# Kernel tuning notes

Hardware: AMD Instinct MI355X
Metric: run time of the kernel (lower is better)

## Reference

```python
import math
import jax, jax.numpy as jnp
import numpy as np

D = 256      # embedding_dim (= internal_dim, downsample_rate 1)
H = 8        # num_heads
HD = D // H  # head_dim = 32
NTC = 16     # num_text_classes
NIMG = 4096  # image tokens (64x64)
N = NIMG + NTC
B = 2
NKE = 64     # num_k_exclude_rope


def _rope(x, freqs):
    # x: (b, h, n, c); freqs: (n, c//2, 2) = (cos, sin) of complex rotary factors
    b, h, n, c = x.shape
    xp = x.reshape(b, h, n, c // 2, 2)
    cos, sin = freqs[..., 0], freqs[..., 1]
    xr, xi = xp[..., 0], xp[..., 1]
    out_r = xr * cos - xi * sin
    out_i = xr * sin + xi * cos
    return jnp.stack([out_r, out_i], axis=-1).reshape(b, h, n, c)


def _sep_heads(x):
    b, n, c = x.shape
    return x.reshape(b, n, H, c // H).transpose(0, 2, 1, 3)  # (b,h,n,hd)


def setup_inputs() -> dict:
    key = jax.random.key(0)
    ks = jax.random.split(key, 14)
    s = 0.02
    # rotary factors: unit-norm cos/sin pairs
    ang_img = jax.random.uniform(ks[3], (NIMG, HD // 2)) * (2.0 * np.pi)
    ang_txt = jax.random.uniform(ks[4], (NTC, HD // 2)) * (2.0 * np.pi)
    return {
        "q": jax.random.normal(ks[0], (B, N, D), dtype=jnp.float32),
        "k": jax.random.normal(ks[1], (B, N, D), dtype=jnp.float32),
        "v": jax.random.normal(ks[2], (B, N, D), dtype=jnp.float32),
        "freqs_cis_img": jnp.stack([jnp.cos(ang_img), jnp.sin(ang_img)], axis=-1),
        "freqs_cis_txt": jnp.stack([jnp.cos(ang_txt), jnp.sin(ang_txt)], axis=-1),
        "Wq": jax.random.normal(ks[5], (D, D), dtype=jnp.float32) * s,
        "bq": jnp.zeros((D,), dtype=jnp.float32),
        "Wk": jax.random.normal(ks[6], (D, D), dtype=jnp.float32) * s,
        "bk": jnp.zeros((D,), dtype=jnp.float32),
        "Wv": jax.random.normal(ks[7], (D, D), dtype=jnp.float32) * s,
        "bv": jnp.zeros((D,), dtype=jnp.float32),
        "Wo": jax.random.normal(ks[8], (D, D), dtype=jnp.float32) * s,
        "bo": jnp.zeros((D,), dtype=jnp.float32),
        "num_k_exclude_rope": NKE,
    }


def reference(q, k, v, freqs_cis_img, freqs_cis_txt,
              Wq, bq, Wk, bk, Wv, bv, Wo, bo, num_k_exclude_rope):
    q = q @ Wq.T + bq
    k = k @ Wk.T + bk
    v = v @ Wv.T + bv
    q = _sep_heads(q)  # (b,h,n,hd)
    k = _sep_heads(k)
    v = _sep_heads(v)

    # split tokens into image / text regions, apply RoPE separately
    q_img, q_txt = q[:, :, :-NTC, :], q[:, :, -NTC:, :]
    k_img, k_txt = k[:, :, :-NTC, :], k[:, :, -NTC:, :]
    q_img = _rope(q_img, freqs_cis_img)
    k_img = _rope(k_img, freqs_cis_img)
    q_txt = _rope(q_txt, freqs_cis_txt)
    k_txt = _rope(k_txt, freqs_cis_txt)
    q = jnp.concatenate([q_img, q_txt], axis=-2)
    k = jnp.concatenate([k_img, k_txt], axis=-2)

    scale = 1.0 / math.sqrt(HD)
    nke = num_k_exclude_rope
    if nke > 0:
        k_td, k_mem = k[:, :, :-nke, :], k[:, :, -nke:, :]
        v_td, v_mem = v[:, :, :-nke, :], v[:, :, -nke:, :]
        attn = jax.nn.softmax(jnp.einsum('bhqd,bhkd->bhqk', q, k_td) * scale, axis=-1)
        out = jnp.einsum('bhqk,bhkd->bhqd', attn, v_td)
        attn_m = jax.nn.softmax(jnp.einsum('bhqd,bhkd->bhqk', q, k_mem) * scale, axis=-1)
        out = out + jnp.einsum('bhqk,bhkd->bhqd', attn_m, v_mem)
    else:
        attn = jax.nn.softmax(jnp.einsum('bhqd,bhkd->bhqk', q, k) * scale, axis=-1)
        out = jnp.einsum('bhqk,bhkd->bhqd', attn, v)

    b, h, n, hd = out.shape
    out = out.transpose(0, 2, 1, 3).reshape(b, n, h * hd)
    return out @ Wo.T + bo
```

## Files before the change

### kernel.cpp

```cpp
#include <hip/hip_runtime.h>
#include <hip/hip_bf16.h>

#define BN    4112
#define NKR   4160
#define BNP   4160
#define BB    2
#define HH    8
#define NIMG_ 4096
#define NMAIN 4048
#define MROWS 8224
#define QSCALE 0.25505402f

typedef __attribute__((ext_vector_type(8))) short short8;
typedef __attribute__((ext_vector_type(4))) float f32x4;
typedef __attribute__((ext_vector_type(16))) float f32x16;

__device__ __forceinline__ unsigned short f2bs(float x) { return __bfloat16_as_ushort(__float2bfloat16(x)); }
__device__ __forceinline__ unsigned pkbf(float a, float b) {
    __hip_bfloat162 h = __float22bfloat162_rn(make_float2(a, b));
    unsigned u; __builtin_memcpy(&u, &h, 4); return u;
}
__device__ __forceinline__ float fexp2(float x) {
#if __has_builtin(__builtin_amdgcn_exp2f)
    return __builtin_amdgcn_exp2f(x);
#else
    return exp2f(x);
#endif
}

__global__ __launch_bounds__(256)
void qkv_mfma(const float* __restrict__ Aq, const float* __restrict__ Ak, const float* __restrict__ Av,
              const float* __restrict__ Wq, const float* __restrict__ Wk, const float* __restrict__ Wv,
              const float* __restrict__ bq, const float* __restrict__ bk, const float* __restrict__ bv,
              short* __restrict__ Qr, short* __restrict__ Kr, short* __restrict__ Vt,
              const float* __restrict__ fimg, const float* __restrict__ ftxt)
{
    __shared__ __align__(16) short Ws[2][64][72];
    __shared__ __align__(16) short Ds[2][64][72];

    const int mode = blockIdx.z;
    const float* A    = (mode == 0) ? Aq : (mode == 1) ? Ak : Av;
    const float* W    = (mode == 0) ? Wq : (mode == 1) ? Wk : Wv;
    const float* bias = (mode == 0) ? bq : (mode == 1) ? bk : bv;

    const int t    = threadIdx.x;
    const int wave = t >> 6, lane = t & 63, q16 = lane & 15, quad = lane >> 4;
    const int f0 = blockIdx.x * 64;
    const int m0 = blockIdx.y * 64;
    const int sr = t >> 2, sc = (t & 3) * 16;
    const int arow = m0 + sr;
    const bool aval = arow < MROWS;
    const float* wp = W + (size_t)(f0 + sr) * 256 + sc;
    const float* ap = A + (size_t)(aval ? arow : 0) * 256 + sc;

    f32x4 acc[4] = {{0,0,0,0},{0,0,0,0},{0,0,0,0},{0,0,0,0}};

    uint4 wr0, wr1, dr0, dr1;
    {
        float4 a0 = *(const float4*)(wp),     a1 = *(const float4*)(wp + 4);
        float4 a2 = *(const float4*)(wp + 8), a3 = *(const float4*)(wp + 12);
        wr0 = uint4{pkbf(a0.x,a0.y), pkbf(a0.z,a0.w), pkbf(a1.x,a1.y), pkbf(a1.z,a1.w)};
        wr1 = uint4{pkbf(a2.x,a2.y), pkbf(a2.z,a2.w), pkbf(a3.x,a3.y), pkbf(a3.z,a3.w)};
        a0 = *(const float4*)(ap);     a1 = *(const float4*)(ap + 4);
        a2 = *(const float4*)(ap + 8); a3 = *(const float4*)(ap + 12);
        dr0 = uint4{pkbf(a0.x,a0.y), pkbf(a0.z,a0.w), pkbf(a1.x,a1.y), pkbf(a1.z,a1.w)};
        dr1 = uint4{pkbf(a2.x,a2.y), pkbf(a2.z,a2.w), pkbf(a3.x,a3.y), pkbf(a3.z,a3.w)};
    }
    *(uint4*)&Ws[0][sr][sc] = wr0; *(uint4*)&Ws[0][sr][sc + 8] = wr1;
    *(uint4*)&Ds[0][sr][sc] = dr0; *(uint4*)&Ds[0][sr][sc + 8] = dr1;
    __syncthreads();

    #pragma unroll
    for (int ki = 0; ki < 4; ++ki) {
        const int buf = ki & 1;
        if (ki < 3) {
            const int k1 = (ki + 1) * 64;
            float4 a0 = *(const float4*)(wp + k1),     a1 = *(const float4*)(wp + k1 + 4);
            float4 a2 = *(const float4*)(wp + k1 + 8), a3 = *(const float4*)(wp + k1 + 12);
            wr0 = uint4{pkbf(a0.x,a0.y), pkbf(a0.z,a0.w), pkbf(a1.x,a1.y), pkbf(a1.z,a1.w)};
            wr1 = uint4{pkbf(a2.x,a2.y), pkbf(a2.z,a2.w), pkbf(a3.x,a3.y), pkbf(a3.z,a3.w)};
            a0 = *(const float4*)(ap + k1);     a1 = *(const float4*)(ap + k1 + 4);
            a2 = *(const float4*)(ap + k1 + 8); a3 = *(const float4*)(ap + k1 + 12);
            dr0 = uint4{pkbf(a0.x,a0.y), pkbf(a0.z,a0.w), pkbf(a1.x,a1.y), pkbf(a1.z,a1.w)};
            dr1 = uint4{pkbf(a2.x,a2.y), pkbf(a2.z,a2.w), pkbf(a3.x,a3.y), pkbf(a3.z,a3.w)};
        }
        #pragma unroll
        for (int ks = 0; ks < 2; ++ks) {
            const short8 af = *(const short8*)&Ws[buf][wave * 16 + q16][ks * 32 + quad * 8];
            #pragma unroll
            for (int ct = 0; ct < 4; ++ct) {
                const short8 bf = *(const short8*)&Ds[buf][ct * 16 + q16][ks * 32 + quad * 8];
                acc[ct] = __builtin_amdgcn_mfma_f32_16x16x32_bf16(af, bf, acc[ct], 0, 0, 0);
            }
        }
        if (ki < 3) {
            *(uint4*)&Ws[buf ^ 1][sr][sc] = wr0; *(uint4*)&Ws[buf ^ 1][sr][sc + 8] = wr1;
            *(uint4*)&Ds[buf ^ 1][sr][sc] = dr0; *(uint4*)&Ds[buf ^ 1][sr][sc + 8] = dr1;
            __syncthreads();
        }
    }

    const int fbase = f0 + wave * 16 + quad * 4;
    const float4 bb = *(const float4*)(bias + fbase);
    float vs[4][4];
    #pragma unroll
    for (int ct = 0; ct < 4; ++ct) {
        int n = m0 + ct * 16 + q16;
        float v0 = acc[ct][0] + bb.x, v1 = acc[ct][1] + bb.y;
        float v2 = acc[ct][2] + bb.z, v3 = acc[ct][3] + bb.w;
        int b  = (n >= BN) ? 1 : 0;
        int nb = n - b * BN;
        if (mode < 2) {
            int j0 = (fbase & 31) >> 1;
            const float* fr = (nb < NIMG_) ? (fimg + ((size_t)nb * 16 + j0) * 2)
                                           : (ftxt + ((size_t)(nb - NIMG_) * 16 + j0) * 2);
            float4 cs = *(const float4*)fr;
            float r0 = v0 * cs.x - v1 * cs.y, i0 = v0 * cs.y + v1 * cs.x;
            float r1 = v2 * cs.z - v3 * cs.w, i1 = v2 * cs.w + v3 * cs.z;
            v0 = r0; v1 = i0; v2 = r1; v3 = i1;
        }
        if (mode == 2) {
            vs[ct][0] = v0; vs[ct][1] = v1; vs[ct][2] = v2; vs[ct][3] = v3;
            continue;
        }
        if (n >= MROWS) continue;
        const int h = (fbase >> 5) & 7, hd = fbase & 31;
        if (mode == 0) {
            unsigned short* op = (unsigned short*)Qr + (((size_t)(b * HH + h) * BN + nb) * 32 + hd);
            *(uint2*)op = uint2{pkbf(v0 * QSCALE, v1 * QSCALE), pkbf(v2 * QSCALE, v3 * QSCALE)};
        } else {
            int nk = nb + ((nb >= NMAIN) ? 48 : 0);
            unsigned short* op = (unsigned short*)Kr + (((size_t)(b * HH + h) * NKR + nk) * 32 + hd);
            *(uint2*)op = uint2{pkbf(v0, v1), pkbf(v2, v3)};
        }
    }

    if (mode == 2) {
        short (*Tr)[72] = Ds[0];
        const int fl = wave * 16 + quad * 4;
        #pragma unroll
        for (int ct = 0; ct < 4; ++ct) {
            const int nl = ct * 16 + q16;
            Tr[fl + 0][nl] = (short)f2bs(vs[ct][0]);
            Tr[fl + 1][nl] = (short)f2bs(vs[ct][1]);
            Tr[fl + 2][nl] = (short)f2bs(vs[ct][2]);
            Tr[fl + 3][nl] = (short)f2bs(vs[ct][3]);
        }
        __syncthreads();
        const int h0 = (f0 >> 5) & 7;
        #pragma unroll
        for (int ii = 0; ii < 2; ++ii) {
            const int r  = ii * 32 + (t >> 3);
            const int c8 = (t & 7) * 8;
            const int ng = m0 + c8;
            if (ng < MROWS) {
                uint4 val = *(const uint4*)&Tr[r][c8];
                int b  = (ng >= BN) ? 1 : 0;
                int nb = ng - b * BN;
                int nk = nb + ((nb >= NMAIN) ? 48 : 0);
                int h  = h0 + (r >> 5), hd = r & 31;
                unsigned short* op = (unsigned short*)Vt + ((size_t)(b * HH + h) * 32 + hd) * BNP + nk;
                *(uint4*)op = val;
            }
        }
    }

    if (blockIdx.x == 0 && blockIdx.y < 16 && t < 192) {
        const int bh = blockIdx.y;
        if (mode == 1) {
            short* base = Kr + (size_t)bh * NKR * 32 + (size_t)NMAIN * 32;
            *(uint4*)(base + t * 8) = uint4{0u, 0u, 0u, 0u};
        } else if (mode == 2) {
            short* base = Vt + (size_t)bh * 32 * BNP + (size_t)(t / 6) * BNP + NMAIN + (t % 6) * 8;
            *(uint4*)base = uint4{0u, 0u, 0u, 0u};
        }
    }
}

__global__ __launch_bounds__(256, 4)
void attn_mfma(const short* __restrict__ Qr, const short* __restrict__ Kr,
               const short* __restrict__ Vt, unsigned short* __restrict__ AO)
{
    __shared__ __align__(16) short Ks[2][2][64][40];
    __shared__ __align__(16) short Vs[2][2][32][72];

    const int t    = threadIdx.x;
    const int wave = t >> 6, lane = t & 63, q32 = lane & 31, hi = lane >> 5;
    const int grp  = wave >> 1, w2 = wave & 1;

    const int b_   = blockIdx.x;
    const int idx  = b_ >> 3;
    const int bh   = ((b_ & 7) << 1) + (idx >= 65 ? 1 : 0);
    const int bx   = idx - (idx >= 65 ? 65 : 0);

    const int q  = bx * 64 + w2 * 32 + q32;
    const int qc = (q < BN) ? q : (BN - 1);
    const short* qp = Qr + ((size_t)bh * BN + qc) * 32 + hi * 8;
    const short8 qf0 = *(const short8*)(qp);
    const short8 qf1 = *(const short8*)(qp + 16);

    f32x16 oAx = {0,0,0,0,0,0,0,0,0,0,0,0,0,0,0,0};
    f32x16 oAy = {0,0,0,0,0,0,0,0,0,0,0,0,0,0,0,0};
    f32x16 oBx = {0,0,0,0,0,0,0,0,0,0,0,0,0,0,0,0};
    const f32x16 z16 = {0,0,0,0,0,0,0,0,0,0,0,0,0,0,0,0};
    float LA = 0.f, LB = 0.f;

    const int tg = t & 127;
    const int kr = tg >> 2, kc = tg & 3;
    const int vr = tg >> 3, vc = tg & 7;
    const short* kg = Kr + (size_t)bh * NKR * 32 + (size_t)grp * 65536 + (size_t)kr * 32 + kc * 8;
    const short* vg = Vt + (size_t)bh * 32 * BNP + (size_t)vr * BNP + grp * 2048
                         + (vc >> 1) * 16 + (vc & 1) * 4;
    const int ntiles = 32 + grp;

    auto tile = [&](int buf, f32x16& ox, f32x16& oy, float& L) {
        const short8 kf00 = *(const short8*)&Ks[grp][buf][q32][hi * 8];
        const short8 kf01 = *(const short8*)&Ks[grp][buf][q32][16 + hi * 8];
        const short8 kf10 = *(const short8*)&Ks[grp][buf][32 + q32][hi * 8];
        const short8 kf11 = *(const short8*)&Ks[grp][buf][32 + q32][16 + hi * 8];
        f32x16 s0 = __builtin_amdgcn_mfma_f32_32x32x16_bf16(kf00, qf0, z16, 0, 0, 0);
        f32x16 s1 = __builtin_amdgcn_mfma_f32_32x32x16_bf16(kf10, qf0, z16, 0, 0, 0);
        s0 = __builtin_amdgcn_mfma_f32_32x32x16_bf16(kf01, qf1, s0, 0, 0, 0);
        s1 = __builtin_amdgcn_mfma_f32_32x32x16_bf16(kf11, qf1, s1, 0, 0, 0);
        float p0[16], p1[16];
        #pragma unroll
        for (int r = 0; r < 16; ++r) p0[r] = fexp2(s0[r]);
        #pragma unroll
        for (int r = 0; r < 16; ++r) p1[r] = fexp2(s1[r]);
        float l0 = (((p0[0]+p0[1])+(p0[2]+p0[3])) + ((p0[4]+p0[5])+(p0[6]+p0[7])))
                 + (((p0[8]+p0[9])+(p0[10]+p0[11])) + ((p0[12]+p0[13])+(p0[14]+p0[15])));
        float l1 = (((p1[0]+p1[1])+(p1[2]+p1[3])) + ((p1[4]+p1[5])+(p1[6]+p1[7])))
                 + (((p1[8]+p1[9])+(p1[10]+p1[11])) + ((p1[12]+p1[13])+(p1[14]+p1[15])));
        #pragma unroll
        for (int m = 0; m < 2; ++m) {
            uint4 pbu = uint4{pkbf(p0[8*m+0], p0[8*m+1]), pkbf(p0[8*m+2], p0[8*m+3]),
                              pkbf(p0[8*m+4], p0[8*m+5]), pkbf(p0[8*m+6], p0[8*m+7])};
            short8 pb; __builtin_memcpy(&pb, &pbu, 16);
            const short8 vf = *(const short8*)&Vs[grp][buf][q32][m * 16 + hi * 8];
            ox = __builtin_amdgcn_mfma_f32_32x32x16_bf16(vf, pb, ox, 0, 0, 0);
        }
        #pragma unroll
        for (int m = 0; m < 2; ++m) {
            uint4 pbu = uint4{pkbf(p1[8*m+0], p1[8*m+1]), pkbf(p1[8*m+2], p1[8*m+3]),
                              pkbf(p1[8*m+4], p1[8*m+5]), pkbf(p1[8*m+6], p1[8*m+7])};
            short8 pb; __builtin_memcpy(&pb, &pbu, 16);
            const short8 vf = *(const short8*)&Vs[grp][buf][q32][32 + m * 16 + hi * 8];
            oy = __builtin_amdgcn_mfma_f32_32x32x16_bf16(vf, pb, oy, 0, 0, 0);
        }
        L += l0 + l1;
    };

    *(uint4*)&Ks[grp][0][kr][kc * 8]      = *(const uint4*)(kg);
    *(uint4*)&Ks[grp][0][kr + 32][kc * 8] = *(const uint4*)(kg + 1024);
    {
        uint2 a0 = *(const uint2*)(vg),              b0 = *(const uint2*)(vg + 8);
        uint2 a1 = *(const uint2*)(vg + 16 * BNP),   b1 = *(const uint2*)(vg + 16 * BNP + 8);
        *(uint4*)&Vs[grp][0][vr][vc * 8]      = uint4{a0.x, a0.y, b0.x, b0.y};
        *(uint4*)&Vs[grp][0][vr + 16][vc * 8] = uint4{a1.x, a1.y, b1.x, b1.y};
    }
    __syncthreads();

    for (int it = 0; it < 33; ++it) {
        const int buf = it & 1;
        uint4 kreg0, kreg1; uint2 va0, vb0, va1, vb1;
        const bool pre = (it + 1) < ntiles;
        if (pre) {
            const short* kp = kg + (size_t)(it + 1) * 2048;
            kreg0 = *(const uint4*)(kp);
            kreg1 = *(const uint4*)(kp + 1024);
            const short* vp = vg + (it + 1) * 64;
            va0 = *(const uint2*)(vp);            vb0 = *(const uint2*)(vp + 8);
            va1 = *(const uint2*)(vp + 16 * BNP); vb1 = *(const uint2*)(vp + 16 * BNP + 8);
        }
        if (it < ntiles) {
            __builtin_amdgcn_s_setprio(1);
            if (grp == 0 || it < 32) tile(buf, oAx, oAy, LA);
            else                     tile(buf, oBx, oBx, LB);
            __builtin_amdgcn_s_setprio(0);
        }
        if (pre) {
            *(uint4*)&Ks[grp][buf ^ 1][kr][kc * 8]      = kreg0;
            *(uint4*)&Ks[grp][buf ^ 1][kr + 32][kc * 8] = kreg1;
            *(uint4*)&Vs[grp][buf ^ 1][vr][vc * 8]      = uint4{va0.x, va0.y, vb0.x, vb0.y};
            *(uint4*)&Vs[grp][buf ^ 1][vr + 16][vc * 8] = uint4{va1.x, va1.y, vb1.x, vb1.y};
        }
        __syncthreads();
    }

    f32x16 oA = oAx + oAy;
    f32x16 oB = oBx;

    LA += __shfl_xor(LA, 32);
    LB += __shfl_xor(LB, 32);

    float* ex = (float*)&Ks[0][0][0][0];
    const int slot = (w2 * 64 + lane) * 20;
    if (grp == 0) {
        #pragma unroll
        for (int i = 0; i < 4; ++i)
            *(f32x4*)(ex + slot + 4 * i) = f32x4{oA[4*i], oA[4*i+1], oA[4*i+2], oA[4*i+3]};
        ex[slot + 16] = LA;
    }
    __syncthreads();

    if (grp == 1 && q < BN) {
        float LT = LA + ex[slot + 16] - 48.f;
        const float iA = 1.f / LT, iB = 1.f / LB;
        const int b = bh >> 3, h = bh & 7;
        unsigned short* ap = AO + ((size_t)b * BN + q) * 256 + h * 32;
        #pragma unroll
        for (int k = 0; k < 4; ++k) {
            f32x4 a = *(const f32x4*)(ex + slot + 4 * k);
            float w0 = (oA[4*k+0] + a[0]) * iA + oB[4*k+0] * iB;
            float w1 = (oA[4*k+1] + a[1]) * iA + oB[4*k+1] * iB;
            float w2 = (oA[4*k+2] + a[2]) * iA + oB[4*k+2] * iB;
            float w3 = (oA[4*k+3] + a[3]) * iA + oB[4*k+3] * iB;
            *(uint2*)(ap + 8 * k + 4 * hi) = uint2{pkbf(w0, w1), pkbf(w2, w3)};
        }
    }
}

__global__ __launch_bounds__(256)
void gemm_out(const unsigned short* __restrict__ A, const float* __restrict__ W,
              const float* __restrict__ bias, float* __restrict__ out)
{
    __shared__ __align__(16) short Ws[2][64][72];
    __shared__ __align__(16) short Ds[2][64][72];
    const int t    = threadIdx.x;
    const int wave = t >> 6, lane = t & 63, q16 = lane & 15, quad = lane >> 4;
    const int f0 = blockIdx.x * 64, m0 = blockIdx.y * 64;
    const int sr = t >> 2, sc = (t & 3) * 16;
    const int arow = m0 + sr;
    const bool aval = arow < MROWS;
    const float* wp = W + (size_t)(f0 + sr) * 256 + sc;
    const unsigned short* ap = A + (size_t)(aval ? arow : 0) * 256 + sc;

    f32x4 acc[4] = {{0,0,0,0},{0,0,0,0},{0,0,0,0},{0,0,0,0}};

    uint4 wr0, wr1, dr0, dr1;
    {
        float4 a0 = *(const float4*)(wp),     a1 = *(const float4*)(wp + 4);
        float4 a2 = *(const float4*)(wp + 8), a3 = *(const float4*)(wp + 12);
        wr0 = uint4{pkbf(a0.x,a0.y), pkbf(a0.z,a0.w), pkbf(a1.x,a1.y), pkbf(a1.z,a1.w)};
        wr1 = uint4{pkbf(a2.x,a2.y), pkbf(a2.z,a2.w), pkbf(a3.x,a3.y), pkbf(a3.z,a3.w)};
        dr0 = *(const uint4*)(ap); dr1 = *(const uint4*)(ap + 8);
    }
    *(uint4*)&Ws[0][sr][sc] = wr0; *(uint4*)&Ws[0][sr][sc + 8] = wr1;
    *(uint4*)&Ds[0][sr][sc] = dr0; *(uint4*)&Ds[0][sr][sc + 8] = dr1;
    __syncthreads();

    #pragma unroll
    for (int ki = 0; ki < 4; ++ki) {
        const int buf = ki & 1;
        if (ki < 3) {
            const int k1 = (ki + 1) * 64;
            float4 a0 = *(const float4*)(wp + k1),     a1 = *(const float4*)(wp + k1 + 4);
            float4 a2 = *(const float4*)(wp + k1 + 8), a3 = *(const float4*)(wp + k1 + 12);
            wr0 = uint4{pkbf(a0.x,a0.y), pkbf(a0.z,a0.w), pkbf(a1.x,a1.y), pkbf(a1.z,a1.w)};
            wr1 = uint4{pkbf(a2.x,a2.y), pkbf(a2.z,a2.w), pkbf(a3.x,a3.y), pkbf(a3.z,a3.w)};
            dr0 = *(const uint4*)(ap + k1); dr1 = *(const uint4*)(ap + k1 + 8);
        }
        #pragma unroll
        for (int ks = 0; ks < 2; ++ks) {
            const short8 af = *(const short8*)&Ws[buf][wave * 16 + q16][ks * 32 + quad * 8];
            #pragma unroll
            for (int ct = 0; ct < 4; ++ct) {
                const short8 bf = *(const short8*)&Ds[buf][ct * 16 + q16][ks * 32 + quad * 8];
                acc[ct] = __builtin_amdgcn_mfma_f32_16x16x32_bf16(af, bf, acc[ct], 0, 0, 0);
            }
        }
        if (ki < 3) {
            *(uint4*)&Ws[buf ^ 1][sr][sc] = wr0; *(uint4*)&Ws[buf ^ 1][sr][sc + 8] = wr1;
            *(uint4*)&Ds[buf ^ 1][sr][sc] = dr0; *(uint4*)&Ds[buf ^ 1][sr][sc + 8] = dr1;
            __syncthreads();
        }
    }

    const int fbase = f0 + wave * 16 + quad * 4;
    const float4 bb = *(const float4*)(bias + fbase);
    #pragma unroll
    for (int ct = 0; ct < 4; ++ct) {
        int n = m0 + ct * 16 + q16;
        if (n >= MROWS) continue;
        float* op = out + (size_t)n * 256 + fbase;
        *(float4*)op = float4{acc[ct][0] + bb.x, acc[ct][1] + bb.y,
                              acc[ct][2] + bb.z, acc[ct][3] + bb.w};
    }
}

extern "C" void kernel_launch(void* const* d_in, const int* in_sizes, int n_in,
                              void* d_out, int out_size, void* d_ws, size_t ws_size,
                              hipStream_t stream)
{
    (void)in_sizes; (void)n_in; (void)out_size; (void)ws_size;
    const float* q    = (const float*)d_in[0];
    const float* k    = (const float*)d_in[1];
    const float* v    = (const float*)d_in[2];
    const float* fimg = (const float*)d_in[3];
    const float* ftxt = (const float*)d_in[4];
    const float* Wq   = (const float*)d_in[5];
    const float* bq   = (const float*)d_in[6];
    const float* Wk   = (const float*)d_in[7];
    const float* bk   = (const float*)d_in[8];
    const float* Wv   = (const float*)d_in[9];
    const float* bv   = (const float*)d_in[10];
    const float* Wo   = (const float*)d_in[11];
    const float* bo   = (const float*)d_in[12];

    char* w = (char*)d_ws;
    short*          Qr = (short*)(w);
    short*          Kr = (short*)(w + 4210688);
    short*          Vt = (short*)(w + 8470528);
    unsigned short* AO = (unsigned short*)(w + 12730368);

    qkv_mfma<<<dim3(4, 129, 3), 256, 0, stream>>>(q, k, v, Wq, Wk, Wv, bq, bk, bv,
                                                  Qr, Kr, Vt, fimg, ftxt);
    attn_mfma<<<dim3(1040), 256, 0, stream>>>(Qr, Kr, Vt, AO);
    gemm_out<<<dim3(4, 129), 256, 0, stream>>>(AO, Wo, bo, (float*)d_out);
}
```

Measured before the change: 193.0 us.

## Give each wave private single-buffered K/V tiles and drop per-iteration block barriers

```diff
diff --git a/kernel.cpp b/kernel.cpp
--- a/kernel.cpp
+++ b/kernel.cpp
@@ -181,43 +181,61 @@
 void attn_mfma(const short* __restrict__ Qr, const short* __restrict__ Kr,
                const short* __restrict__ Vt, unsigned short* __restrict__ AO)
 {
-    __shared__ __align__(16) short Ks[2][2][64][40];
-    __shared__ __align__(16) short Vs[2][2][32][72];
+    __shared__ __align__(16) short Ks[4][64][40];
+    __shared__ __align__(16) short Vs[4][32][72];
 
     const int t    = threadIdx.x;
     const int wave = t >> 6, lane = t & 63, q32 = lane & 31, hi = lane >> 5;
-    const int grp  = wave >> 1, w2 = wave & 1;
+    const int grp  = wave & 1;
+    const int qg   = wave >> 1;
 
     const int b_   = blockIdx.x;
     const int idx  = b_ >> 3;
     const int bh   = ((b_ & 7) << 1) + (idx >= 65 ? 1 : 0);
     const int bx   = idx - (idx >= 65 ? 65 : 0);
 
-    const int q  = bx * 64 + w2 * 32 + q32;
+    const int q  = bx * 64 + qg * 32 + q32;
     const int qc = (q < BN) ? q : (BN - 1);
     const short* qp = Qr + ((size_t)bh * BN + qc) * 32 + hi * 8;
     const short8 qf0 = *(const short8*)(qp);
     const short8 qf1 = *(const short8*)(qp + 16);
 
-    f32x16 oAx = {0,0,0,0,0,0,0,0,0,0,0,0,0,0,0,0};
-    f32x16 oAy = {0,0,0,0,0,0,0,0,0,0,0,0,0,0,0,0};
-    f32x16 oBx = {0,0,0,0,0,0,0,0,0,0,0,0,0,0,0,0};
+    f32x16 oA = {0,0,0,0,0,0,0,0,0,0,0,0,0,0,0,0};
+    f32x16 oB = {0,0,0,0,0,0,0,0,0,0,0,0,0,0,0,0};
     const f32x16 z16 = {0,0,0,0,0,0,0,0,0,0,0,0,0,0,0,0};
     float LA = 0.f, LB = 0.f;
 
-    const int tg = t & 127;
-    const int kr = tg >> 2, kc = tg & 3;
-    const int vr = tg >> 3, vc = tg & 7;
-    const short* kg = Kr + (size_t)bh * NKR * 32 + (size_t)grp * 65536 + (size_t)kr * 32 + kc * 8;
-    const short* vg = Vt + (size_t)bh * 32 * BNP + (size_t)vr * BNP + grp * 2048
-                         + (vc >> 1) * 16 + (vc & 1) * 4;
-    const int ntiles = 32 + grp;
-
-    auto tile = [&](int buf, f32x16& ox, f32x16& oy, float& L) {
-        const short8 kf00 = *(const short8*)&Ks[grp][buf][q32][hi * 8];
-        const short8 kf01 = *(const short8*)&Ks[grp][buf][q32][16 + hi * 8];
-        const short8 kf10 = *(const short8*)&Ks[grp][buf][32 + q32][hi * 8];
-        const short8 kf11 = *(const short8*)&Ks[grp][buf][32 + q32][16 + hi * 8];
+    const int krow = lane >> 1, khalf = lane & 1;
+    const int vrow = lane >> 2, vseg = lane & 3;
+    const short* kgb = Kr + (size_t)bh * NKR * 32 + (size_t)grp * 65536
+                          + (size_t)krow * 32 + khalf * 16;
+    const short* vgb = Vt + (size_t)bh * 32 * BNP + (size_t)vrow * BNP + grp * 2048 + vseg * 16;
+
+    short (*KsW)[40] = Ks[wave];
+    short (*VsW)[72] = Vs[wave];
+
+    auto commit = [&](uint4 k0, uint4 k1, uint4 k2, uint4 k3,
+                      uint4 vl0, uint4 vh0, uint4 vl1, uint4 vh1) {
+        *(uint4*)&KsW[krow][khalf * 16]          = k0;
+        *(uint4*)&KsW[krow][khalf * 16 + 8]      = k1;
+        *(uint4*)&KsW[krow + 32][khalf * 16]     = k2;
+        *(uint4*)&KsW[krow + 32][khalf * 16 + 8] = k3;
+        *(uint4*)&VsW[vrow][vseg * 16]           = uint4{vl0.x, vl0.y, vh0.x, vh0.y};
+        *(uint4*)&VsW[vrow][vseg * 16 + 8]       = uint4{vl0.z, vl0.w, vh0.z, vh0.w};
+        *(uint4*)&VsW[vrow + 16][vseg * 16]      = uint4{vl1.x, vl1.y, vh1.x, vh1.y};
+        *(uint4*)&VsW[vrow + 16][vseg * 16 + 8]  = uint4{vl1.z, vl1.w, vh1.z, vh1.w};
+    };
+
+    auto tileC = [&](f32x16& o, float& L) {
+        const short8 kf00 = *(const short8*)&KsW[q32][hi * 8];
+        const short8 kf01 = *(const short8*)&KsW[q32][16 + hi * 8];
+        const short8 kf10 = *(const short8*)&KsW[32 + q32][hi * 8];
+        const short8 kf11 = *(const short8*)&KsW[32 + q32][16 + hi * 8];
+        const short8 vf0 = *(const short8*)&VsW[q32][hi * 8];
+        const short8 vf1 = *(const short8*)&VsW[q32][16 + hi * 8];
+        const short8 vf2 = *(const short8*)&VsW[q32][32 + hi * 8];
+        const short8 vf3 = *(const short8*)&VsW[q32][48 + hi * 8];
+        __builtin_amdgcn_s_setprio(1);
         f32x16 s0 = __builtin_amdgcn_mfma_f32_32x32x16_bf16(kf00, qf0, z16, 0, 0, 0);
         f32x16 s1 = __builtin_amdgcn_mfma_f32_32x32x16_bf16(kf10, qf0, z16, 0, 0, 0);
         s0 = __builtin_amdgcn_mfma_f32_32x32x16_bf16(kf01, qf1, s0, 0, 0, 0);
@@ -231,86 +249,79 @@
                  + (((p0[8]+p0[9])+(p0[10]+p0[11])) + ((p0[12]+p0[13])+(p0[14]+p0[15])));
         float l1 = (((p1[0]+p1[1])+(p1[2]+p1[3])) + ((p1[4]+p1[5])+(p1[6]+p1[7])))
                  + (((p1[8]+p1[9])+(p1[10]+p1[11])) + ((p1[12]+p1[13])+(p1[14]+p1[15])));
-        #pragma unroll
-        for (int m = 0; m < 2; ++m) {
-            uint4 pbu = uint4{pkbf(p0[8*m+0], p0[8*m+1]), pkbf(p0[8*m+2], p0[8*m+3]),
-                              pkbf(p0[8*m+4], p0[8*m+5]), pkbf(p0[8*m+6], p0[8*m+7])};
+        {
+            uint4 pbu = uint4{pkbf(p0[0], p0[1]), pkbf(p0[2], p0[3]),
+                              pkbf(p0[4], p0[5]), pkbf(p0[6], p0[7])};
             short8 pb; __builtin_memcpy(&pb, &pbu, 16);
-            const short8 vf = *(const short8*)&Vs[grp][buf][q32][m * 16 + hi * 8];
-            ox = __builtin_amdgcn_mfma_f32_32x32x16_bf16(vf, pb, ox, 0, 0, 0);
-        }
-        #pragma unroll
-        for (int m = 0; m < 2; ++m) {
-            uint4 pbu = uint4{pkbf(p1[8*m+0], p1[8*m+1]), pkbf(p1[8*m+2], p1[8*m+3]),
-                              pkbf(p1[8*m+4], p1[8*m+5]), pkbf(p1[8*m+6], p1[8*m+7])};
+            o = __builtin_amdgcn_mfma_f32_32x32x16_bf16(vf0, pb, o, 0, 0, 0);
+        }
+        {
+            uint4 pbu = uint4{pkbf(p0[8], p0[9]),  pkbf(p0[10], p0[11]),
+                              pkbf(p0[12], p0[13]), pkbf(p0[14], p0[15])};
             short8 pb; __builtin_memcpy(&pb, &pbu, 16);
-            const short8 vf = *(const short8*)&Vs[grp][buf][q32][32 + m * 16 + hi * 8];
-            oy = __builtin_amdgcn_mfma_f32_32x32x16_bf16(vf, pb, oy, 0, 0, 0);
-        }
+            o = __builtin_amdgcn_mfma_f32_32x32x16_bf16(vf1, pb, o, 0, 0, 0);
+        }
+        {
+            uint4 pbu = uint4{pkbf(p1[0], p1[1]), pkbf(p1[2], p1[3]),
+                              pkbf(p1[4], p1[5]), pkbf(p1[6], p1[7])};
+            short8 pb; __builtin_memcpy(&pb, &pbu, 16);
+            o = __builtin_amdgcn_mfma_f32_32x32x16_bf16(vf2, pb, o, 0, 0, 0);
+        }
+        {
+            uint4 pbu = uint4{pkbf(p1[8], p1[9]),  pkbf(p1[10], p1[11]),
+                              pkbf(p1[12], p1[13]), pkbf(p1[14], p1[15])};
+            short8 pb; __builtin_memcpy(&pb, &pbu, 16);
+            o = __builtin_amdgcn_mfma_f32_32x32x16_bf16(vf3, pb, o, 0, 0, 0);
+        }
+        __builtin_amdgcn_s_setprio(0);
         L += l0 + l1;
     };
 
-    *(uint4*)&Ks[grp][0][kr][kc * 8]      = *(const uint4*)(kg);
-    *(uint4*)&Ks[grp][0][kr + 32][kc * 8] = *(const uint4*)(kg + 1024);
     {
-        uint2 a0 = *(const uint2*)(vg),              b0 = *(const uint2*)(vg + 8);
-        uint2 a1 = *(const uint2*)(vg + 16 * BNP),   b1 = *(const uint2*)(vg + 16 * BNP + 8);
-        *(uint4*)&Vs[grp][0][vr][vc * 8]      = uint4{a0.x, a0.y, b0.x, b0.y};
-        *(uint4*)&Vs[grp][0][vr + 16][vc * 8] = uint4{a1.x, a1.y, b1.x, b1.y};
-    }
-    __syncthreads();
-
-    for (int it = 0; it < 33; ++it) {
-        const int buf = it & 1;
-        uint4 kreg0, kreg1; uint2 va0, vb0, va1, vb1;
-        const bool pre = (it + 1) < ntiles;
+        uint4 k0 = *(const uint4*)(kgb),        k1 = *(const uint4*)(kgb + 8);
+        uint4 k2 = *(const uint4*)(kgb + 1024), k3 = *(const uint4*)(kgb + 1024 + 8);
+        uint4 vl0 = *(const uint4*)(vgb),            vh0 = *(const uint4*)(vgb + 8);
+        uint4 vl1 = *(const uint4*)(vgb + 16 * BNP), vh1 = *(const uint4*)(vgb + 16 * BNP + 8);
+        commit(k0, k1, k2, k3, vl0, vh0, vl1, vh1);
+    }
+
+    for (int it = 0; it < 32; ++it) {
+        uint4 k0, k1, k2, k3, vl0, vh0, vl1, vh1;
+        const bool pre = (it + 1 < 32) || (grp == 1 && it == 31);
         if (pre) {
-            const short* kp = kg + (size_t)(it + 1) * 2048;
-            kreg0 = *(const uint4*)(kp);
-            kreg1 = *(const uint4*)(kp + 1024);
-            const short* vp = vg + (it + 1) * 64;
-            va0 = *(const uint2*)(vp);            vb0 = *(const uint2*)(vp + 8);
-            va1 = *(const uint2*)(vp + 16 * BNP); vb1 = *(const uint2*)(vp + 16 * BNP + 8);
-        }
-        if (it < ntiles) {
-            __builtin_amdgcn_s_setprio(1);
-            if (grp == 0 || it < 32) tile(buf, oAx, oAy, LA);
-            else                     tile(buf, oBx, oBx, LB);
-            __builtin_amdgcn_s_setprio(0);
-        }
-        if (pre) {
-            *(uint4*)&Ks[grp][buf ^ 1][kr][kc * 8]      = kreg0;
-            *(uint4*)&Ks[grp][buf ^ 1][kr + 32][kc * 8] = kreg1;
-            *(uint4*)&Vs[grp][buf ^ 1][vr][vc * 8]      = uint4{va0.x, va0.y, vb0.x, vb0.y};
-            *(uint4*)&Vs[grp][buf ^ 1][vr + 16][vc * 8] = uint4{va1.x, va1.y, vb1.x, vb1.y};
-        }
-        __syncthreads();
-    }
-
-    f32x16 oA = oAx + oAy;
-    f32x16 oB = oBx;
+            const short* kp = kgb + (size_t)(it + 1) * 2048;
+            k0 = *(const uint4*)(kp);        k1 = *(const uint4*)(kp + 8);
+            k2 = *(const uint4*)(kp + 1024); k3 = *(const uint4*)(kp + 1024 + 8);
+            const short* vp = vgb + (it + 1) * 64;
+            vl0 = *(const uint4*)(vp);            vh0 = *(const uint4*)(vp + 8);
+            vl1 = *(const uint4*)(vp + 16 * BNP); vh1 = *(const uint4*)(vp + 16 * BNP + 8);
+        }
+        tileC(oA, LA);
+        if (pre) commit(k0, k1, k2, k3, vl0, vh0, vl1, vh1);
+    }
+    if (grp == 1) tileC(oB, LB);
 
     LA += __shfl_xor(LA, 32);
     LB += __shfl_xor(LB, 32);
 
-    float* ex = (float*)&Ks[0][0][0][0];
-    const int slot = (w2 * 64 + lane) * 20;
+    float* exw = (float*)&Ks[qg << 1][0][0];
+    const int slot = lane * 20;
     if (grp == 0) {
         #pragma unroll
         for (int i = 0; i < 4; ++i)
-            *(f32x4*)(ex + slot + 4 * i) = f32x4{oA[4*i], oA[4*i+1], oA[4*i+2], oA[4*i+3]};
-        ex[slot + 16] = LA;
+            *(f32x4*)(exw + slot + 4 * i) = f32x4{oA[4*i], oA[4*i+1], oA[4*i+2], oA[4*i+3]};
+        exw[slot + 16] = LA;
     }
     __syncthreads();
 
     if (grp == 1 && q < BN) {
-        float LT = LA + ex[slot + 16] - 48.f;
+        float LT = LA + exw[slot + 16] - 48.f;
         const float iA = 1.f / LT, iB = 1.f / LB;
         const int b = bh >> 3, h = bh & 7;
         unsigned short* ap = AO + ((size_t)b * BN + q) * 256 + h * 32;
         #pragma unroll
         for (int k = 0; k < 4; ++k) {
-            f32x4 a = *(const f32x4*)(ex + slot + 4 * k);
+            f32x4 a = *(const f32x4*)(exw + slot + 4 * k);
             float w0 = (oA[4*k+0] + a[0]) * iA + oB[4*k+0] * iB;
             float w1 = (oA[4*k+1] + a[1]) * iA + oB[4*k+1] * iB;
             float w2 = (oA[4*k+2] + a[2]) * iA + oB[4*k+2] * iB;
```

After: 247.0 us. +28.0%, slower.
